# Kernel optimization log

Hardware: AMD Instinct MI355X
Metric: run time of the kernel (lower is better)

## Reference

```python
import jax, jax.numpy as jnp
import numpy as np

B, S_ENC, S_DEC, D_IN, UNITS = 8, 2048, 1024, 512, 512

def setup_inputs() -> dict:
    key = jax.random.key(0)
    k1, k2, k3, k4, k5 = jax.random.split(key, 5)
    scale = 1.0 / np.sqrt(D_IN)
    return {
        "encoding": jax.random.normal(k1, (B, S_ENC, D_IN), dtype=jnp.float32),
        "decoding": jax.random.normal(k2, (B, S_DEC, D_IN), dtype=jnp.float32),
        "Wq": jax.random.normal(k3, (D_IN, UNITS), dtype=jnp.float32) * scale,
        "Wk": jax.random.normal(k4, (D_IN, UNITS), dtype=jnp.float32) * scale,
        "Wv": jax.random.normal(k5, (D_IN, UNITS), dtype=jnp.float32) * scale,
    }

def reference(encoding, decoding, Wq, Wk, Wv):
    # bias-free projections
    q = jnp.einsum('bsd,du->bsu', decoding, Wq)   # [B, S_dec, U]
    k = jnp.einsum('bsd,du->bsu', encoding, Wk)   # [B, S_enc, U]
    v = jnp.einsum('bsd,du->bsu', encoding, Wv)   # [B, S_enc, U]
    # NOTE: original applies no 1/sqrt(d) scaling
    score = jnp.einsum('bqu,bku->bqk', q, k)      # [B, S_dec, S_enc]
    score = jax.nn.softmax(score, axis=2)
    return jnp.einsum('bqk,bku->bqu', score, v)   # [B, S_dec, U]
```

## Files before the change

kernel.cpp:

```cpp
#include <hip/hip_runtime.h>
#include <hip/hip_bf16.h>


typedef __attribute__((ext_vector_type(8))) _Float16 f16x8;
typedef __attribute__((ext_vector_type(4))) _Float16 f16x4;
typedef __attribute__((ext_vector_type(4))) float f32x4;

#define MFMA16(a, b, c) __builtin_amdgcn_mfma_f32_16x16x32_f16(a, b, c, 0, 0, 0)
#define L2E 1.44269504088896f

__device__ __forceinline__ void glds16(const void* g, void* l) {
    __builtin_amdgcn_global_load_lds(
        (const __attribute__((address_space(1))) void*)g,
        (__attribute__((address_space(3))) void*)l, 16, 0, 0);
}

__global__ __launch_bounds__(256) void prep_kernel(
    const float* __restrict__ enc, const float* __restrict__ dec,
    const float* __restrict__ Wq, const float* __restrict__ Wk,
    const float* __restrict__ Wv, _Float16* __restrict__ oenc,
    _Float16* __restrict__ odec, _Float16* __restrict__ planes) {
    const int bid = blockIdx.x;
    if (bid < 6144) {
        const float* x;
        _Float16* o;
        size_t i;
        if (bid < 4096) { x = enc; o = oenc; i = ((size_t)bid * 256 + threadIdx.x) * 8; }
        else { x = dec; o = odec; i = ((size_t)(bid - 4096) * 256 + threadIdx.x) * 8; }
        float4 a0 = *(const float4*)(x + i);
        float4 a1 = *(const float4*)(x + i + 4);
        float v[8] = {a0.x, a0.y, a0.z, a0.w, a1.x, a1.y, a1.z, a1.w};
        f16x8 h;
#pragma unroll
        for (int j = 0; j < 8; ++j) h[j] = (_Float16)v[j];
        *(f16x8*)(o + i) = h;
        return;
    }
    const int t = bid - 6144;
    const int zw = t >> 6, r = t & 63;
    const int u0 = (r & 7) * 64, d0 = (r >> 3) * 64;
    const float* W = zw == 0 ? Wq : (zw == 1 ? Wk : Wv);
    _Float16* ot = planes + (size_t)zw * 262144;
    __shared__ float T[64][65];
    const int tr = threadIdx.x >> 4, tc = (threadIdx.x & 15) * 4;
#pragma unroll
    for (int j = 0; j < 4; ++j) {
        float4 vv = *(const float4*)(W + (size_t)(d0 + tr + j * 16) * 512 + u0 + tc);
        T[tr + j * 16][tc + 0] = vv.x;
        T[tr + j * 16][tc + 1] = vv.y;
        T[tr + j * 16][tc + 2] = vv.z;
        T[tr + j * 16][tc + 3] = vv.w;
    }
    __syncthreads();
#pragma unroll
    for (int j = 0; j < 4; ++j) {
        int ul = tr + j * 16;
        f16x4 h;
#pragma unroll
        for (int i = 0; i < 4; ++i) h[i] = (_Float16)T[tc + i][ul];
        *(f16x4*)(ot + (size_t)(u0 + ul) * 512 + d0 + tc) = h;
    }
}

__global__ __launch_bounds__(256) void proj_kernel(
    const _Float16* __restrict__ dech, const _Float16* __restrict__ ench,
    const _Float16* __restrict__ wts, _Float16* __restrict__ qh,
    _Float16* __restrict__ kh, _Float16* __restrict__ vt) {
    __shared__ __align__(16) char smem[40960];
    const int bid = blockIdx.x;
    int seg, bx, by;
    if (bid < 256) { seg = 0; by = bid & 127; bx = bid >> 7; }
    else if (bid < 768) { int t = bid - 256; seg = 1; by = t & 255; bx = t >> 8; }
    else { int t = bid - 768; seg = 2; by = t & 255; bx = t >> 8; }
    const _Float16* A = seg == 0 ? dech : ench;
    const _Float16* Bp = wts + (size_t)seg * 262144;

    const int tid = threadIdx.x;
    const int wave = tid >> 6, lane = tid & 63;
    const int quad = lane >> 4, m16 = lane & 15;
    const int wr = wave >> 1, wc = wave & 1;
    const int row0 = by * 64, col0 = bx * 256;

    const int scol = ((lane & 3) ^ ((lane >> 3) & 3)) * 8;
    const int srowA = wave * 16 + (lane >> 2);
    const int srowB = wave * 64 + (lane >> 2);
    const _Float16* agp = A + (size_t)(row0 + srowA) * 512 + scol;
    const _Float16* bgp = Bp + (size_t)(col0 + srowB) * 512 + scol;
    const int ldsAoff = wave * 1024;
    const int ldsBoff = 4096 + wave * 4096;

    f32x4 acc[2][8];
#pragma unroll
    for (int mt = 0; mt < 2; ++mt)
#pragma unroll
        for (int nt = 0; nt < 8; ++nt) acc[mt][nt] = (f32x4){0.f, 0.f, 0.f, 0.f};

    auto stage = [&](int i, int buf) {
        char* base = smem + buf * 20480;
        const int k0 = i * 32;
        glds16(agp + k0, base + ldsAoff);
#pragma unroll
        for (int j = 0; j < 4; ++j)
            glds16(bgp + k0 + j * 16 * 512, base + ldsBoff + j * 1024);
    };

    const int csw = (quad ^ ((lane >> 1) & 3)) * 16;

    stage(0, 0);
    for (int i = 0; i < 16; ++i) {
        __builtin_amdgcn_s_barrier();
        if (i + 1 < 16) {
            stage(i + 1, (i + 1) & 1);
            asm volatile("s_waitcnt vmcnt(5)" ::: "memory");
        } else {
            asm volatile("s_waitcnt vmcnt(0)" ::: "memory");
        }
        __builtin_amdgcn_s_barrier();
        const char* bb = smem + (i & 1) * 20480;
        const char* pa = bb + (wr * 32 + m16) * 64 + csw;
        const char* pb = bb + 4096 + (wc * 128 + m16) * 64 + csw;
        f16x8 af[2];
#pragma unroll
        for (int mt = 0; mt < 2; ++mt) af[mt] = *(const f16x8*)(pa + mt * 1024);
#pragma unroll
        for (int nt = 0; nt < 8; ++nt) {
            f16x8 bf = *(const f16x8*)(pb + nt * 1024);
#pragma unroll
            for (int mt = 0; mt < 2; ++mt) acc[mt][nt] = MFMA16(af[mt], bf, acc[mt][nt]);
        }
    }

    if (seg < 2) {
        _Float16* o = seg == 0 ? qh : kh;
#pragma unroll
        for (int mt = 0; mt < 2; ++mt)
#pragma unroll
            for (int nt = 0; nt < 8; ++nt)
#pragma unroll
                for (int rr = 0; rr < 4; ++rr) {
                    int row = row0 + wr * 32 + mt * 16 + quad * 4 + rr;
                    int col = col0 + wc * 128 + nt * 16 + m16;
                    o[(size_t)row * 512 + col] = (_Float16)acc[mt][nt][rr];
                }
    } else {
        __syncthreads();
        char* reg = smem + wave * 8192;
#pragma unroll
        for (int nt = 0; nt < 8; ++nt)
#pragma unroll
            for (int mt = 0; mt < 2; ++mt) {
                f16x4 pk;
#pragma unroll
                for (int rr = 0; rr < 4; ++rr) pk[rr] = (_Float16)acc[mt][nt][rr];
                *(f16x4*)(reg + (nt * 16 + m16) * 64 + (mt * 16 + quad * 4) * 2) = pk;
            }
        const int b = row0 >> 11;
        const int s_base = (row0 & 2047) + wr * 32;
        const int u_base = col0 + wc * 128;
        __syncthreads();
#pragma unroll
        for (int j = 0; j < 8; ++j) {
            int n = j * 16 + (lane >> 2);
            int mo = (lane & 3) * 8;
            f16x8 val = *(const f16x8*)(reg + n * 64 + mo * 2);
            *(f16x8*)(vt + (size_t)(b * 512 + u_base + n) * 2048 + s_base + mo) = val;
        }
    }
}

__global__ __launch_bounds__(256) void score_kernel(
    const _Float16* __restrict__ qh, const _Float16* __restrict__ kh,
    float* __restrict__ S) {
    __shared__ __align__(16) char smem[32768];
    const int b = blockIdx.x;
    const int z = b & 7, r = b >> 3;
    const int by = r >> 4, bx = r & 15;
    const int tid = threadIdx.x;
    const int wave = tid >> 6, lane = tid & 63;
    const int quad = lane >> 4, m16 = lane & 15;
    const int wr = wave >> 1, wc = wave & 1;
    const int row0 = z * 1024 + by * 128;
    const int col0 = bx * 128;

    const int scol = ((lane & 3) ^ ((lane >> 3) & 3)) * 8;
    const int srow = wave * 32 + (lane >> 2);
    const _Float16* agp = qh + (size_t)(row0 + srow) * 512 + scol;
    const _Float16* bgp = kh + (size_t)(z * 2048 + col0 + srow) * 512 + scol;
    const int ldsAoff = wave * 2048;
    const int ldsBoff = 8192 + wave * 2048;

    f32x4 acc[4][4];
#pragma unroll
    for (int mt = 0; mt < 4; ++mt)
#pragma unroll
        for (int nt = 0; nt < 4; ++nt) acc[mt][nt] = (f32x4){0.f, 0.f, 0.f, 0.f};

    auto stage = [&](int i, int buf) {
        char* base = smem + buf * 16384;
        const int k0 = i * 32;
#pragma unroll
        for (int j = 0; j < 2; ++j) {
            glds16(agp + k0 + j * 16 * 512, base + ldsAoff + j * 1024);
            glds16(bgp + k0 + j * 16 * 512, base + ldsBoff + j * 1024);
        }
    };

    const int csw = (quad ^ ((lane >> 1) & 3)) * 16;

    stage(0, 0);
    for (int i = 0; i < 16; ++i) {
        __builtin_amdgcn_s_barrier();
        if (i + 1 < 16) {
            stage(i + 1, (i + 1) & 1);
            asm volatile("s_waitcnt vmcnt(4)" ::: "memory");
        } else {
            asm volatile("s_waitcnt vmcnt(0)" ::: "memory");
        }
        __builtin_amdgcn_s_barrier();
        const char* bb = smem + (i & 1) * 16384;
        const char* pa = bb + (wr * 64 + m16) * 64 + csw;
        const char* pb = bb + 8192 + (wc * 64 + m16) * 64 + csw;
        f16x8 af[4];
#pragma unroll
        for (int mt = 0; mt < 4; ++mt) af[mt] = *(const f16x8*)(pa + mt * 1024);
#pragma unroll
        for (int nt = 0; nt < 4; ++nt) {
            f16x8 bf = *(const f16x8*)(pb + nt * 1024);
#pragma unroll
            for (int mt = 0; mt < 4; ++mt) acc[mt][nt] = MFMA16(af[mt], bf, acc[mt][nt]);
        }
    }
#pragma unroll
    for (int mt = 0; mt < 4; ++mt)
#pragma unroll
        for (int nt = 0; nt < 4; ++nt)
#pragma unroll
            for (int rr = 0; rr < 4; ++rr) {
                int row = row0 + wr * 64 + mt * 16 + quad * 4 + rr;
                int col = col0 + wc * 64 + nt * 16 + m16;
                S[(size_t)row * 2048 + col] = acc[mt][nt][rr];
            }
}

__global__ __launch_bounds__(256) void softmax_kernel(const float* __restrict__ S,
                                                      _Float16* __restrict__ P) {
    const int row = blockIdx.x;
    const int tid = threadIdx.x;
    const int wave = tid >> 6, lane = tid & 63;
    __shared__ float red[8];

    const float* sp = S + (size_t)row * 2048 + tid * 8;
    float4 x0 = *(const float4*)sp;
    float4 x1 = *(const float4*)(sp + 4);
    float v[8] = {x0.x, x0.y, x0.z, x0.w, x1.x, x1.y, x1.z, x1.w};

    float mx = v[0];
#pragma unroll
    for (int i = 1; i < 8; ++i) mx = fmaxf(mx, v[i]);
#pragma unroll
    for (int off = 32; off > 0; off >>= 1) mx = fmaxf(mx, __shfl_down(mx, off));
    if (lane == 0) red[wave] = mx;
    __syncthreads();
    if (tid == 0) red[4] = fmaxf(fmaxf(red[0], red[1]), fmaxf(red[2], red[3]));
    __syncthreads();
    mx = red[4];

    float e[8];
    float sum = 0.f;
#pragma unroll
    for (int i = 0; i < 8; ++i) {
        e[i] = exp2f((v[i] - mx) * L2E);
        sum += e[i];
    }
#pragma unroll
    for (int off = 32; off > 0; off >>= 1) sum += __shfl_down(sum, off);
    if (lane == 0) red[wave] = sum;
    __syncthreads();
    if (tid == 0) red[5] = red[0] + red[1] + red[2] + red[3];
    __syncthreads();
    float inv = 1.0f / red[5];

    f16x8 ov;
#pragma unroll
    for (int i = 0; i < 8; ++i) ov[i] = (_Float16)(e[i] * inv);
    *(f16x8*)(P + (size_t)row * 2048 + tid * 8) = ov;
}

__global__ __launch_bounds__(256) void pv_kernel(
    const _Float16* __restrict__ P, const _Float16* __restrict__ vt,
    float* __restrict__ out) {
    __shared__ __align__(16) char smem[24576];
    const int b = blockIdx.x;
    const int z = b & 7, r = b >> 3;
    const int by = r >> 2, bx = r & 3;
    const int tid = threadIdx.x;
    const int wave = tid >> 6, lane = tid & 63;
    const int quad = lane >> 4, m16 = lane & 15;
    const int wr = wave >> 1, wc = wave & 1;
    const int row0 = z * 1024 + by * 64;
    const int col0 = bx * 128;

    const int scol = ((lane & 3) ^ ((lane >> 3) & 3)) * 8;
    const int srowA = wave * 16 + (lane >> 2);
    const int srowB = wave * 32 + (lane >> 2);
    const _Float16* agp = P + (size_t)(row0 + srowA) * 2048 + scol;
    const _Float16* bgp = vt + (size_t)(z * 512 + col0 + srowB) * 2048 + scol;
    const int ldsAoff = wave * 1024;
    const int ldsBoff = 4096 + wave * 2048;

    f32x4 acc[2][4];
#pragma unroll
    for (int mt = 0; mt < 2; ++mt)
#pragma unroll
        for (int nt = 0; nt < 4; ++nt) acc[mt][nt] = (f32x4){0.f, 0.f, 0.f, 0.f};

    auto stage = [&](int i, int buf) {
        char* base = smem + buf * 12288;
        const int k0 = i * 32;
        glds16(agp + k0, base + ldsAoff);
#pragma unroll
        for (int j = 0; j < 2; ++j)
            glds16(bgp + k0 + j * 16 * 2048, base + ldsBoff + j * 1024);
    };

    const int csw = (quad ^ ((lane >> 1) & 3)) * 16;

    stage(0, 0);
    for (int i = 0; i < 64; ++i) {
        __builtin_amdgcn_s_barrier();
        if (i + 1 < 64) {
            stage(i + 1, (i + 1) & 1);
            asm volatile("s_waitcnt vmcnt(3)" ::: "memory");
        } else {
            asm volatile("s_waitcnt vmcnt(0)" ::: "memory");
        }
        __builtin_amdgcn_s_barrier();
        const char* bb = smem + (i & 1) * 12288;
        const char* pa = bb + (wr * 32 + m16) * 64 + csw;
        const char* pb = bb + 4096 + (wc * 64 + m16) * 64 + csw;
        f16x8 af[2];
#pragma unroll
        for (int mt = 0; mt < 2; ++mt) af[mt] = *(const f16x8*)(pa + mt * 1024);
#pragma unroll
        for (int nt = 0; nt < 4; ++nt) {
            f16x8 bf = *(const f16x8*)(pb + nt * 1024);
#pragma unroll
            for (int mt = 0; mt < 2; ++mt) acc[mt][nt] = MFMA16(af[mt], bf, acc[mt][nt]);
        }
    }

#pragma unroll
    for (int mt = 0; mt < 2; ++mt)
#pragma unroll
        for (int nt = 0; nt < 4; ++nt)
#pragma unroll
            for (int rr = 0; rr < 4; ++rr) {
                int row = row0 + wr * 32 + mt * 16 + quad * 4 + rr;
                int col = col0 + wc * 64 + nt * 16 + m16;
                out[(size_t)row * 512 + col] = acc[mt][nt][rr];
            }
}

extern "C" void kernel_launch(void* const* d_in, const int* in_sizes, int n_in,
                              void* d_out, int out_size, void* d_ws, size_t ws_size,
                              hipStream_t stream) {
    const float* enc = (const float*)d_in[0];
    const float* dec = (const float*)d_in[1];
    const float* Wq = (const float*)d_in[2];
    const float* Wk = (const float*)d_in[3];
    const float* Wv = (const float*)d_in[4];
    float* out = (float*)d_out;

    char* ws = (char*)d_ws;
    _Float16* qh = (_Float16*)(ws);
    _Float16* kh = (_Float16*)(ws + ((size_t)8 << 20));
    _Float16* P = (_Float16*)(ws);
    _Float16* vt = (_Float16*)(ws + ((size_t)32 << 20));
    float* S = (float*)(ws + ((size_t)48 << 20));
    _Float16* dech = (_Float16*)(ws + ((size_t)48 << 20));
    _Float16* wts = (_Float16*)(ws + ((size_t)56 << 20));
    _Float16* ench = (_Float16*)(ws + ((size_t)112 << 20));

    dim3 blk(256);
    prep_kernel<<<6336, blk, 0, stream>>>(enc, dec, Wq, Wk, Wv, ench, dech, wts);
    proj_kernel<<<1280, blk, 0, stream>>>(dech, ench, wts, qh, kh, vt);
    score_kernel<<<1024, blk, 0, stream>>>(qh, kh, S);
    softmax_kernel<<<8192, blk, 0, stream>>>(S, P);
    pv_kernel<<<512, blk, 0, stream>>>(P, vt, out);
}
```

Baseline: 198.8 us.

## Fuse score GEMM and softmax into one kernel holding full rows in registers

Replaces the separate score kernel, with its fp32 S write, and the softmax kernel with a single kernel. Each 512-thread block computes a 32-row by 2048-column score tile, with each wave holding 256 columns in registers. Max and sum are reduced through shared memory and normalized fp16 P is written directly. This removes the fp32 S round trip through HBM and one launch. In exchange, K is read straight from global memory without LDS staging, the grid shrinks to 256 blocks, register pressure is high, and the scalar 2-byte P stores are uncoalesced.

```diff
diff --git a/kernel.cpp b/kernel.cpp
--- a/kernel.cpp
+++ b/kernel.cpp
@@ -168,122 +168,140 @@
     }
 }
 
-__global__ __launch_bounds__(256) void score_kernel(
+__global__ __launch_bounds__(512) void score_softmax_kernel(
     const _Float16* __restrict__ qh, const _Float16* __restrict__ kh,
-    float* __restrict__ S) {
-    __shared__ __align__(16) char smem[32768];
-    const int b = blockIdx.x;
-    const int z = b & 7, r = b >> 3;
-    const int by = r >> 4, bx = r & 15;
+    _Float16* __restrict__ P) {
+    __shared__ __align__(16) char smem[35072];
+    const int bid = blockIdx.x;
+    const int batch = bid & 7, qt = bid >> 3;
+    const int row0 = batch * 1024 + qt * 32;
     const int tid = threadIdx.x;
     const int wave = tid >> 6, lane = tid & 63;
     const int quad = lane >> 4, m16 = lane & 15;
-    const int wr = wave >> 1, wc = wave & 1;
-    const int row0 = z * 1024 + by * 128;
-    const int col0 = bx * 128;
-
-    const int scol = ((lane & 3) ^ ((lane >> 3) & 3)) * 8;
-    const int srow = wave * 32 + (lane >> 2);
-    const _Float16* agp = qh + (size_t)(row0 + srow) * 512 + scol;
-    const _Float16* bgp = kh + (size_t)(z * 2048 + col0 + srow) * 512 + scol;
-    const int ldsAoff = wave * 2048;
-    const int ldsBoff = 8192 + wave * 2048;
-
-    f32x4 acc[4][4];
-#pragma unroll
-    for (int mt = 0; mt < 4; ++mt)
-#pragma unroll
-        for (int nt = 0; nt < 4; ++nt) acc[mt][nt] = (f32x4){0.f, 0.f, 0.f, 0.f};
-
-    auto stage = [&](int i, int buf) {
-        char* base = smem + buf * 16384;
-        const int k0 = i * 32;
-#pragma unroll
-        for (int j = 0; j < 2; ++j) {
-            glds16(agp + k0 + j * 16 * 512, base + ldsAoff + j * 1024);
-            glds16(bgp + k0 + j * 16 * 512, base + ldsBoff + j * 1024);
-        }
-    };
-
-    const int csw = (quad ^ ((lane >> 1) & 3)) * 16;
-
-    stage(0, 0);
-    for (int i = 0; i < 16; ++i) {
-        __builtin_amdgcn_s_barrier();
-        if (i + 1 < 16) {
-            stage(i + 1, (i + 1) & 1);
-            asm volatile("s_waitcnt vmcnt(4)" ::: "memory");
-        } else {
-            asm volatile("s_waitcnt vmcnt(0)" ::: "memory");
-        }
-        __builtin_amdgcn_s_barrier();
-        const char* bb = smem + (i & 1) * 16384;
-        const char* pa = bb + (wr * 64 + m16) * 64 + csw;
-        const char* pb = bb + 8192 + (wc * 64 + m16) * 64 + csw;
-        f16x8 af[4];
-#pragma unroll
-        for (int mt = 0; mt < 4; ++mt) af[mt] = *(const f16x8*)(pa + mt * 1024);
-#pragma unroll
-        for (int nt = 0; nt < 4; ++nt) {
-            f16x8 bf = *(const f16x8*)(pb + nt * 1024);
-#pragma unroll
-            for (int mt = 0; mt < 4; ++mt) acc[mt][nt] = MFMA16(af[mt], bf, acc[mt][nt]);
-        }
-    }
-#pragma unroll
-    for (int mt = 0; mt < 4; ++mt)
-#pragma unroll
-        for (int nt = 0; nt < 4; ++nt)
+
+    {
+        const int scol = ((lane & 3) ^ ((lane >> 3) & 3)) * 8;
+#pragma unroll
+        for (int t = 0; t < 2; ++t) {
+            const int d = wave * 2 + t;
+#pragma unroll
+            for (int j = 0; j < 2; ++j) {
+                const int srow = j * 16 + (lane >> 2);
+                glds16(qh + (size_t)(row0 + srow) * 512 + d * 32 + scol,
+                       smem + d * 2048 + j * 1024);
+            }
+        }
+    }
+    __syncthreads();
+
+    f32x4 acc[2][16];
+#pragma unroll
+    for (int mt = 0; mt < 2; ++mt)
+#pragma unroll
+        for (int nt = 0; nt < 16; ++nt) acc[mt][nt] = (f32x4){0.f, 0.f, 0.f, 0.f};
+
+    const int kb = wave * 256;
+    const _Float16* __restrict__ kbase =
+        kh + (size_t)(batch * 2048 + kb + m16) * 512 + quad * 8;
+    const int csw = (quad ^ ((m16 >> 1) & 3)) * 16;
+
+    for (int d = 0; d < 16; ++d) {
+        const char* pa = smem + d * 2048 + m16 * 64 + csw;
+        f16x8 a0 = *(const f16x8*)(pa);
+        f16x8 a1 = *(const f16x8*)(pa + 1024);
+#pragma unroll
+        for (int nt = 0; nt < 16; ++nt) {
+            f16x8 bf = *(const f16x8*)(kbase + nt * 16 * 512 + d * 32);
+            acc[0][nt] = MFMA16(a0, bf, acc[0][nt]);
+            acc[1][nt] = MFMA16(a1, bf, acc[1][nt]);
+        }
+    }
+
+    float rmax[2][4];
+#pragma unroll
+    for (int mt = 0; mt < 2; ++mt)
+#pragma unroll
+        for (int rr = 0; rr < 4; ++rr) {
+            float m = acc[mt][0][rr];
+#pragma unroll
+            for (int nt = 1; nt < 16; ++nt) m = fmaxf(m, acc[mt][nt][rr]);
+#pragma unroll
+            for (int off = 1; off < 16; off <<= 1) m = fmaxf(m, __shfl_xor(m, off));
+            rmax[mt][rr] = m;
+        }
+    float* maxp = (float*)(smem + 32768);
+    float* gmax = (float*)(smem + 33792);
+    float* sump = (float*)(smem + 33920);
+    float* ginv = (float*)(smem + 34944);
+    if (m16 == 0) {
+#pragma unroll
+        for (int mt = 0; mt < 2; ++mt)
+#pragma unroll
+            for (int rr = 0; rr < 4; ++rr)
+                maxp[wave * 32 + mt * 16 + quad * 4 + rr] = rmax[mt][rr];
+    }
+    __syncthreads();
+    if (tid < 32) {
+        float g = maxp[tid];
+#pragma unroll
+        for (int w = 1; w < 8; ++w) g = fmaxf(g, maxp[w * 32 + tid]);
+        gmax[tid] = g;
+    }
+    __syncthreads();
+    float gm[2][4];
+#pragma unroll
+    for (int mt = 0; mt < 2; ++mt)
+#pragma unroll
+        for (int rr = 0; rr < 4; ++rr) gm[mt][rr] = gmax[mt * 16 + quad * 4 + rr];
+    float rsum[2][4];
+#pragma unroll
+    for (int mt = 0; mt < 2; ++mt)
+#pragma unroll
+        for (int rr = 0; rr < 4; ++rr) rsum[mt][rr] = 0.f;
+#pragma unroll
+    for (int mt = 0; mt < 2; ++mt)
+#pragma unroll
+        for (int nt = 0; nt < 16; ++nt)
 #pragma unroll
             for (int rr = 0; rr < 4; ++rr) {
-                int row = row0 + wr * 64 + mt * 16 + quad * 4 + rr;
-                int col = col0 + wc * 64 + nt * 16 + m16;
-                S[(size_t)row * 2048 + col] = acc[mt][nt][rr];
+                float e = exp2f((acc[mt][nt][rr] - gm[mt][rr]) * L2E);
+                acc[mt][nt][rr] = e;
+                rsum[mt][rr] += e;
             }
-}
-
-__global__ __launch_bounds__(256) void softmax_kernel(const float* __restrict__ S,
-                                                      _Float16* __restrict__ P) {
-    const int row = blockIdx.x;
-    const int tid = threadIdx.x;
-    const int wave = tid >> 6, lane = tid & 63;
-    __shared__ float red[8];
-
-    const float* sp = S + (size_t)row * 2048 + tid * 8;
-    float4 x0 = *(const float4*)sp;
-    float4 x1 = *(const float4*)(sp + 4);
-    float v[8] = {x0.x, x0.y, x0.z, x0.w, x1.x, x1.y, x1.z, x1.w};
-
-    float mx = v[0];
-#pragma unroll
-    for (int i = 1; i < 8; ++i) mx = fmaxf(mx, v[i]);
-#pragma unroll
-    for (int off = 32; off > 0; off >>= 1) mx = fmaxf(mx, __shfl_down(mx, off));
-    if (lane == 0) red[wave] = mx;
-    __syncthreads();
-    if (tid == 0) red[4] = fmaxf(fmaxf(red[0], red[1]), fmaxf(red[2], red[3]));
-    __syncthreads();
-    mx = red[4];
-
-    float e[8];
-    float sum = 0.f;
-#pragma unroll
-    for (int i = 0; i < 8; ++i) {
-        e[i] = exp2f((v[i] - mx) * L2E);
-        sum += e[i];
-    }
-#pragma unroll
-    for (int off = 32; off > 0; off >>= 1) sum += __shfl_down(sum, off);
-    if (lane == 0) red[wave] = sum;
-    __syncthreads();
-    if (tid == 0) red[5] = red[0] + red[1] + red[2] + red[3];
-    __syncthreads();
-    float inv = 1.0f / red[5];
-
-    f16x8 ov;
-#pragma unroll
-    for (int i = 0; i < 8; ++i) ov[i] = (_Float16)(e[i] * inv);
-    *(f16x8*)(P + (size_t)row * 2048 + tid * 8) = ov;
+#pragma unroll
+    for (int mt = 0; mt < 2; ++mt)
+#pragma unroll
+        for (int rr = 0; rr < 4; ++rr) {
+#pragma unroll
+            for (int off = 1; off < 16; off <<= 1)
+                rsum[mt][rr] += __shfl_xor(rsum[mt][rr], off);
+        }
+    if (m16 == 0) {
+#pragma unroll
+        for (int mt = 0; mt < 2; ++mt)
+#pragma unroll
+            for (int rr = 0; rr < 4; ++rr)
+                sump[wave * 32 + mt * 16 + quad * 4 + rr] = rsum[mt][rr];
+    }
+    __syncthreads();
+    if (tid < 32) {
+        float s = sump[tid];
+#pragma unroll
+        for (int w = 1; w < 8; ++w) s += sump[w * 32 + tid];
+        ginv[tid] = 1.0f / s;
+    }
+    __syncthreads();
+#pragma unroll
+    for (int mt = 0; mt < 2; ++mt)
+#pragma unroll
+        for (int rr = 0; rr < 4; ++rr) {
+            const float iv = ginv[mt * 16 + quad * 4 + rr];
+            const size_t ro =
+                (size_t)(row0 + mt * 16 + quad * 4 + rr) * 2048 + kb + m16;
+#pragma unroll
+            for (int nt = 0; nt < 16; ++nt)
+                P[ro + nt * 16] = (_Float16)(acc[mt][nt][rr] * iv);
+        }
 }
 
 __global__ __launch_bounds__(256) void pv_kernel(
@@ -374,9 +392,8 @@
     char* ws = (char*)d_ws;
     _Float16* qh = (_Float16*)(ws);
     _Float16* kh = (_Float16*)(ws + ((size_t)8 << 20));
-    _Float16* P = (_Float16*)(ws);
     _Float16* vt = (_Float16*)(ws + ((size_t)32 << 20));
-    float* S = (float*)(ws + ((size_t)48 << 20));
+    _Float16* P = (_Float16*)(ws + ((size_t)48 << 20));
     _Float16* dech = (_Float16*)(ws + ((size_t)48 << 20));
     _Float16* wts = (_Float16*)(ws + ((size_t)56 << 20));
     _Float16* ench = (_Float16*)(ws + ((size_t)112 << 20));
@@ -384,7 +401,6 @@
     dim3 blk(256);
     prep_kernel<<<6336, blk, 0, stream>>>(enc, dec, Wq, Wk, Wv, ench, dech, wts);
     proj_kernel<<<1280, blk, 0, stream>>>(dech, ench, wts, qh, kh, vt);
-    score_kernel<<<1024, blk, 0, stream>>>(qh, kh, S);
-    softmax_kernel<<<8192, blk, 0, stream>>>(S, P);
+    score_softmax_kernel<<<256, dim3(512), 0, stream>>>(qh, kh, P);
     pv_kernel<<<512, blk, 0, stream>>>(P, vt, out);
 }
```

Measured after the change: 229.9 us. 1.16x slower.
